# Optimization experiments

Measured on AMD Instinct MI355X. Metric: run time of the kernel, lower is better.

Reference implementation:

```python
import jax, jax.numpy as jnp
import numpy as np

N_NODES = 200000
IN_SIZE = 128
OUT_SIZE = 128
N_EDGES = 600000


def setup_inputs() -> dict:
    key = jax.random.key(0)
    k1, k2, k3, k4 = jax.random.split(key, 4)
    embedding = jax.random.normal(k1, (N_NODES, IN_SIZE), dtype=jnp.float32)
    up2down_edge_index = jax.random.randint(k2, (2, N_EDGES), 0, N_NODES, dtype=jnp.int64)
    # GCNConv params (glorot weight, zero bias as in PyG defaults)
    scale = np.sqrt(6.0 / (IN_SIZE + OUT_SIZE)).astype(np.float32)
    W = jax.random.uniform(k3, (IN_SIZE, OUT_SIZE), dtype=jnp.float32, minval=-scale, maxval=scale)
    b = jnp.zeros((OUT_SIZE,), dtype=jnp.float32)
    return {"embedding": embedding, "up2down_edge_index": up2down_edge_index, "W": W, "b": b}


def reference(embedding, up2down_edge_index, W, b):
    # PyG GCNConv: add self-loops, symmetric normalization, linear transform,
    # scatter-sum aggregation, add bias.
    N = embedding.shape[0]
    loops = jnp.arange(N, dtype=up2down_edge_index.dtype)
    src = jnp.concatenate([up2down_edge_index[0], loops])  # message sources
    dst = jnp.concatenate([up2down_edge_index[1], loops])  # message targets

    # degree of each target node (edge_weight = 1)
    deg = jax.ops.segment_sum(jnp.ones_like(src, dtype=embedding.dtype), dst, num_segments=N)
    deg_inv_sqrt = jnp.where(deg > 0, jax.lax.rsqrt(jnp.maximum(deg, 1.0)), 0.0)
    norm = deg_inv_sqrt[src] * deg_inv_sqrt[dst]  # [E+N]

    h = embedding @ W  # [N, out]
    msg = h[src] * norm[:, None]  # gather + scale, [E+N, out]
    out = jax.ops.segment_sum(msg, dst, num_segments=N)  # scatter-add
    return out + b
```

## Files before the change

### kernel.cpp

```cpp
#include <hip/hip_runtime.h>
#include <hip/hip_bf16.h>
#include <stdint.h>

typedef __attribute__((ext_vector_type(8))) short short8v;
typedef __attribute__((ext_vector_type(4))) float f32x4;

__device__ __forceinline__ unsigned short f2bf(float f) {
  unsigned int u = __float_as_uint(f);
  u += 0x7fffu + ((u >> 16) & 1u);
  return (unsigned short)(u >> 16);
}
__device__ __forceinline__ unsigned int pack2bf(float a, float b) {
  return (unsigned int)f2bf(a) | ((unsigned int)f2bf(b) << 16);
}
__device__ __forceinline__ float bf_lo(unsigned int v) { return __uint_as_float(v << 16); }
__device__ __forceinline__ float bf_hi(unsigned int v) { return __uint_as_float(v & 0xffff0000u); }

__global__ void k_prep(uint4* __restrict__ zp, int n16,
                       const float* __restrict__ W, unsigned short* __restrict__ Wfrag) {
  int b = blockIdx.x;
  if (b < 64) {
    int t = b * 256 + threadIdx.x;
    int j = t & 7;
    int lane = (t >> 3) & 63;
    int ktct = t >> 9;
    int kt = ktct & 3, ct = ktct >> 2;
    int col = ct * 16 + (lane & 15);
    int k = kt * 32 + 4 * (lane >> 4) + (j & 3) + 16 * (j >> 2);
    Wfrag[t] = f2bf(W[k * 128 + col]);
  } else {
    int i = (b - 64) * 256 + threadIdx.x;
    if (i < n16) {
      uint4 z; z.x = z.y = z.z = z.w = 0u;
      zp[i] = z;
    }
  }
}

__global__ void k_count(const int* __restrict__ dst, int* deg, int E) {
  int e = blockIdx.x * blockDim.x + threadIdx.x;
  if (e < E) atomicAdd(&deg[dst[e]], 1);
}

__global__ void k_blocksum(const int* __restrict__ deg, int* partials, float* dis, int N) {
  __shared__ int s[256];
  int t = threadIdx.x;
  int i = blockIdx.x * 256 + t;
  int c = (i < N) ? deg[i] : 0;
  if (i < N) dis[i] = rsqrtf((float)(c + 1));
  s[t] = c;
  __syncthreads();
  for (int off = 128; off > 0; off >>= 1) {
    if (t < off) s[t] += s[t + off];
    __syncthreads();
  }
  if (t == 0) partials[blockIdx.x] = s[0];
}

__global__ void k_scan_final2(const int* __restrict__ deg, const int* __restrict__ partials,
                              int* csr_off, int N, int E) {
  __shared__ int s[256];
  __shared__ int base;
  int t = threadIdx.x;
  int accp = 0;
  for (int j = t; j < blockIdx.x; j += 256) accp += partials[j];
  s[t] = accp;
  __syncthreads();
  for (int off = 128; off > 0; off >>= 1) {
    if (t < off) s[t] += s[t + off];
    __syncthreads();
  }
  if (t == 0) base = s[0];
  __syncthreads();
  int i = blockIdx.x * 256 + t;
  int c = (i < N) ? deg[i] : 0;
  s[t] = c;
  __syncthreads();
  for (int off = 1; off < 256; off <<= 1) {
    int v = (t >= off) ? s[t - off] : 0;
    __syncthreads();
    s[t] += v;
    __syncthreads();
  }
  if (i < N) csr_off[i] = base + s[t] - c;
  if (i == 0) csr_off[N] = E;
}

__global__ void k_fill(const int* __restrict__ src, const int* __restrict__ dst,
                       const int* __restrict__ csr_off, int* cursor, int* csr_src, int E) {
  int e = blockIdx.x * blockDim.x + threadIdx.x;
  if (e < E) {
    int d = dst[e];
    int p = atomicAdd(&cursor[d], 1);
    csr_src[csr_off[d] + p] = src[e];
  }
}

__device__ __forceinline__ short8v pack8(f32x4 a, f32x4 b) {
  short8v r;
  r[0] = (short)f2bf(a[0]); r[1] = (short)f2bf(a[1]);
  r[2] = (short)f2bf(a[2]); r[3] = (short)f2bf(a[3]);
  r[4] = (short)f2bf(b[0]); r[5] = (short)f2bf(b[1]);
  r[6] = (short)f2bf(b[2]); r[7] = (short)f2bf(b[3]);
  return r;
}


#define GLOAD(XB, DD, TT, HAS)                                                  \
  do {                                                                          \
    if (HAS) {                                                                  \
      int row_ = (TT) * 16 + lr;                                                \
      if (row_ < N) {                                                           \
        const float* xp_ = X + (size_t)row_ * 128 + 4 * lg;                     \
        _Pragma("unroll") for (int q = 0; q < 4; ++q) {                         \
          XB[2 * q]     = *(const f32x4*)(xp_ + q * 32);                        \
          XB[2 * q + 1] = *(const f32x4*)(xp_ + q * 32 + 16);                   \
        }                                                                       \
        DD = dis[row_];                                                         \
      } else {                                                                  \
        _Pragma("unroll") for (int q = 0; q < 8; ++q) {                         \
          XB[q][0] = XB[q][1] = XB[q][2] = XB[q][3] = 0.f;                      \
        }                                                                       \
        DD = 0.f;                                                               \
      }                                                                         \
    }                                                                           \
  } while (0)

#define GCOMPUTE(XB, DD, TT)                                                    \
  do {                                                                          \
    short8v afr[4];                                                             \
    _Pragma("unroll") for (int kt = 0; kt < 4; ++kt)                            \
        afr[kt] = pack8(XB[2 * kt], XB[2 * kt + 1]);                            \
    int row_ = (TT) * 16 + lr;                                                  \
    bool wr_ = row_ < N;                                                        \
    unsigned short* hp_ = hs + (size_t)row_ * 128;                              \
    float dd_ = DD;                                                             \
    _Pragma("unroll") for (int cp = 0; cp < 4; ++cp) {                          \
      f32x4 a0 = {0.f, 0.f, 0.f, 0.f}, a1 = {0.f, 0.f, 0.f, 0.f};               \
      _Pragma("unroll") for (int kt = 0; kt < 4; ++kt)                          \
          a0 = __builtin_amdgcn_mfma_f32_16x16x32_bf16(wreg[(2 * cp) * 4 + kt], \
                                                       afr[kt], a0, 0, 0, 0);   \
      _Pragma("unroll") for (int kt = 0; kt < 4; ++kt)                          \
          a1 = __builtin_amdgcn_mfma_f32_16x16x32_bf16(                         \
              wreg[(2 * cp + 1) * 4 + kt], afr[kt], a1, 0, 0, 0);               \
      unsigned int u0x = pack2bf(a0[0] * dd_, a0[1] * dd_);                     \
      unsigned int u0y = pack2bf(a0[2] * dd_, a0[3] * dd_);                     \
      unsigned int u1x = pack2bf(a1[0] * dd_, a1[1] * dd_);                     \
      unsigned int u1y = pack2bf(a1[2] * dd_, a1[3] * dd_);                     \
      int s_ = lg & 1;                                                          \
      unsigned int sx = s_ ? u0x : u1x, sy = s_ ? u0y : u1y;                    \
      unsigned int rx = (unsigned int)__shfl_xor((int)sx, 16);                  \
      unsigned int ry = (unsigned int)__shfl_xor((int)sy, 16);                  \
      uint4 uu;                                                                 \
      if (s_ == 0) { uu.x = u0x; uu.y = u0y; uu.z = rx; uu.w = ry; }            \
      else         { uu.x = rx; uu.y = ry; uu.z = u1x; uu.w = u1y; }            \
      int cb = (s_ ? (2 * cp + 1) : (2 * cp)) * 16 + 8 * (lg >> 1);             \
      if (wr_) *(uint4*)(hp_ + cb) = uu;                                        \
    }                                                                           \
  } while (0)

__global__ __launch_bounds__(256, 2) void k_gemm5(const float* __restrict__ X,
     const unsigned short* __restrict__ Wfrag, const float* __restrict__ dis,
     unsigned short* __restrict__ hs, int N, int ntile) {
  int lane = threadIdx.x & 63;
  int gw = (blockIdx.x * blockDim.x + threadIdx.x) >> 6;
  int nw = (gridDim.x * blockDim.x) >> 6;
  int lr = lane & 15, lg = lane >> 4;

  short8v wreg[32];
  #pragma unroll
  for (int f = 0; f < 32; ++f)
    wreg[f] = *(const short8v*)(Wfrag + (size_t)(f * 64 + lane) * 8);

  int tile = gw;
  if (tile >= ntile) return;

  f32x4 xv[8], nx[8];
  float d0 = 0.f, d1 = 0.f;
  GLOAD(xv, d0, tile, true);

  for (;;) {
    int t1 = tile + nw;
    bool h1 = t1 < ntile;
    GLOAD(nx, d1, t1, h1);
    __builtin_amdgcn_sched_barrier(0);
    GCOMPUTE(xv, d0, tile);
    if (!h1) break;
    int t2 = t1 + nw;
    bool h2 = t2 < ntile;
    GLOAD(xv, d0, t2, h2);
    __builtin_amdgcn_sched_barrier(0);
    GCOMPUTE(nx, d1, t1);
    if (!h2) break;
    tile = t2;
  }
}

__device__ __forceinline__ void acc8(float* a, uint4 g) {
  a[0] += bf_lo(g.x); a[1] += bf_hi(g.x);
  a[2] += bf_lo(g.y); a[3] += bf_hi(g.y);
  a[4] += bf_lo(g.z); a[5] += bf_hi(g.z);
  a[6] += bf_lo(g.w); a[7] += bf_hi(g.w);
}

__global__ __launch_bounds__(256) void k_agg2(const unsigned short* __restrict__ hs_,
     const int* __restrict__ csr_src, const int* __restrict__ csr_off,
     const float* __restrict__ dis, const float* __restrict__ bias,
     float* __restrict__ out, int N) {
  const uint4* hs = (const uint4*)hs_;
  int lane = threadIdx.x & 63;
  int c = lane & 15;
  int base = lane & 48;
  int gid = (blockIdx.x * blockDim.x + threadIdx.x) >> 4;
  int G = (gridDim.x * blockDim.x) >> 4;
  int i0 = (int)(((long long)gid * N) / G);
  int i1 = (int)(((long long)(gid + 1) * N) / G);
  if (i0 >= i1) return;
  float4 bA = ((const float4*)bias)[c * 2];
  float4 bB = ((const float4*)bias)[c * 2 + 1];
  int e1prev = csr_off[i0];
  for (int i = i0; i < i1; ++i) {
    int e0 = e1prev;
    int e1 = csr_off[i + 1];
    e1prev = e1;
    float a[8];
    uint4 sv = hs[(size_t)i * 16 + c];
    a[0] = bf_lo(sv.x); a[1] = bf_hi(sv.x);
    a[2] = bf_lo(sv.y); a[3] = bf_hi(sv.y);
    a[4] = bf_lo(sv.z); a[5] = bf_hi(sv.z);
    a[6] = bf_lo(sv.w); a[7] = bf_hi(sv.w);
    int e = e0;
    while (e < e1) {
      int p = e + c;
      int myidx = (p < e1) ? csr_src[p] : 0;
      int kb = (e1 - e < 16) ? (e1 - e) : 16;
      int k = 0;
      for (; k + 8 <= kb; k += 8) {
        int s[8];
        #pragma unroll
        for (int q = 0; q < 8; ++q) s[q] = __shfl(myidx, base + k + q);
        uint4 g[8];
        #pragma unroll
        for (int q = 0; q < 8; ++q) g[q] = hs[(size_t)s[q] * 16 + c];
        #pragma unroll
        for (int q = 0; q < 8; ++q) acc8(a, g[q]);
      }
      for (; k < kb; k += 4) {
        int s0 = __shfl(myidx, base + k);
        int s1 = __shfl(myidx, base + k + 1);
        int s2 = __shfl(myidx, base + k + 2);
        int s3 = __shfl(myidx, base + k + 3);
        bool v1 = (k + 1 < kb), v2 = (k + 2 < kb), v3 = (k + 3 < kb);
        uint4 g0 = hs[(size_t)s0 * 16 + c];
        uint4 g1 = hs[(size_t)(v1 ? s1 : i) * 16 + c];
        uint4 g2 = hs[(size_t)(v2 ? s2 : i) * 16 + c];
        uint4 g3 = hs[(size_t)(v3 ? s3 : i) * 16 + c];
        if (!v1) { g1.x = g1.y = g1.z = g1.w = 0u; }
        if (!v2) { g2.x = g2.y = g2.z = g2.w = 0u; }
        if (!v3) { g3.x = g3.y = g3.z = g3.w = 0u; }
        acc8(a, g0); acc8(a, g1); acc8(a, g2); acc8(a, g3);
      }
      e += kb;
    }
    float di = dis[i];
    f32x4 o0, o1;
    o0[0] = fmaf(di, a[0], bA.x); o0[1] = fmaf(di, a[1], bA.y);
    o0[2] = fmaf(di, a[2], bA.z); o0[3] = fmaf(di, a[3], bA.w);
    o1[0] = fmaf(di, a[4], bB.x); o1[1] = fmaf(di, a[5], bB.y);
    o1[2] = fmaf(di, a[6], bB.z); o1[3] = fmaf(di, a[7], bB.w);
    f32x4* op = (f32x4*)(out + (size_t)i * 128);
    __builtin_nontemporal_store(o0, op + c * 2);
    __builtin_nontemporal_store(o1, op + c * 2 + 1);
  }
}

extern "C" void kernel_launch(void* const* d_in, const int* in_sizes, int n_in,
                              void* d_out, int out_size, void* d_ws, size_t ws_size,
                              hipStream_t stream) {
  const float* X    = (const float*)d_in[0];
  const int*   edge = (const int*)d_in[1];
  const float* W    = (const float*)d_in[2];
  const float* bias = (const float*)d_in[3];
  float* out = (float*)d_out;
  int N = in_sizes[0] / 128;
  int E = in_sizes[1] / 2;
  const int* srcArr = edge;
  const int* dstArr = edge + E;

  char* w = (char*)d_ws;
  auto align = [](size_t x) { return (x + 255) & ~(size_t)255; };
  size_t o = 0;
  int*   deg      = (int*)(w + o);   o += align((size_t)N * 4);
  int*   cursor   = (int*)(w + o);   o += align((size_t)N * 4);
  float* dis      = (float*)(w + o); o += align((size_t)N * 4);
  int*   csr_off  = (int*)(w + o);   o += align(((size_t)N + 1) * 4);
  int*   csr_src  = (int*)(w + o);   o += align((size_t)E * 4);
  int*   partials = (int*)(w + o);   o += align((size_t)4096 * 4);
  unsigned short* Wfrag = (unsigned short*)(w + o); o += align((size_t)16384 * 2);
  unsigned short* hs    = (unsigned short*)(w + o);

  int nbN = (N + 255) / 256;
  int nbE = (E + 255) / 256;
  int ntile = (N + 15) / 16;

  size_t zbytes = align((size_t)N * 4) + align((size_t)N * 4);
  int n16 = (int)(zbytes / 16);
  k_prep<<<64 + (n16 + 255) / 256, 256, 0, stream>>>((uint4*)deg, n16, W, Wfrag);
  k_count<<<nbE, 256, 0, stream>>>(dstArr, deg, E);
  k_blocksum<<<nbN, 256, 0, stream>>>(deg, partials, dis, N);
  k_scan_final2<<<nbN, 256, 0, stream>>>(deg, partials, csr_off, N, E);
  k_fill<<<nbE, 256, 0, stream>>>(srcArr, dstArr, csr_off, cursor, csr_src, E);
  k_gemm5<<<512, 256, 0, stream>>>(X, Wfrag, dis, hs, N, ntile);
  k_agg2<<<4096, 256, 0, stream>>>(hs, csr_src, csr_off, dis, bias, out, N);
}
```

Baseline: 149.0 us.

## Fuse block-sum into count kernel and triple-buffer GEMM tile loads

The per-block degree partial sums are now built with a second atomic during edge counting, which removes the separate block-sum kernel and one launch. The rsqrt degree normalisation moves into the scan kernel. Partials move into the zeroed workspace region. The GEMM loop changes from double to triple buffering of X tiles to deepen load prefetch, at the cost of more registers and extra contended atomics on the partials array.

```diff
diff --git a/kernel.cpp b/kernel.cpp
--- a/kernel.cpp
+++ b/kernel.cpp
@@ -37,28 +37,17 @@
   }
 }
 
-__global__ void k_count(const int* __restrict__ dst, int* deg, int E) {
+__global__ void k_count2(const int* __restrict__ dst, int* deg, int* partials, int E) {
   int e = blockIdx.x * blockDim.x + threadIdx.x;
-  if (e < E) atomicAdd(&deg[dst[e]], 1);
-}
-
-__global__ void k_blocksum(const int* __restrict__ deg, int* partials, float* dis, int N) {
-  __shared__ int s[256];
-  int t = threadIdx.x;
-  int i = blockIdx.x * 256 + t;
-  int c = (i < N) ? deg[i] : 0;
-  if (i < N) dis[i] = rsqrtf((float)(c + 1));
-  s[t] = c;
-  __syncthreads();
-  for (int off = 128; off > 0; off >>= 1) {
-    if (t < off) s[t] += s[t + off];
-    __syncthreads();
-  }
-  if (t == 0) partials[blockIdx.x] = s[0];
-}
-
-__global__ void k_scan_final2(const int* __restrict__ deg, const int* __restrict__ partials,
-                              int* csr_off, int N, int E) {
+  if (e < E) {
+    int d = dst[e];
+    atomicAdd(&deg[d], 1);
+    atomicAdd(&partials[d >> 8], 1);
+  }
+}
+
+__global__ void k_scan_final3(const int* __restrict__ deg, const int* __restrict__ partials,
+                              int* csr_off, float* __restrict__ dis, int N, int E) {
   __shared__ int s[256];
   __shared__ int base;
   int t = threadIdx.x;
@@ -74,6 +63,7 @@
   __syncthreads();
   int i = blockIdx.x * 256 + t;
   int c = (i < N) ? deg[i] : 0;
+  if (i < N) dis[i] = rsqrtf((float)(c + 1));
   s[t] = c;
   __syncthreads();
   for (int off = 1; off < 256; off <<= 1) {
@@ -172,27 +162,36 @@
   for (int f = 0; f < 32; ++f)
     wreg[f] = *(const short8v*)(Wfrag + (size_t)(f * 64 + lane) * 8);
 
-  int tile = gw;
-  if (tile >= ntile) return;
-
-  f32x4 xv[8], nx[8];
-  float d0 = 0.f, d1 = 0.f;
-  GLOAD(xv, d0, tile, true);
+  int t0 = gw;
+  if (t0 >= ntile) return;
+
+  f32x4 b0[8], b1[8], b2[8];
+  float d0 = 0.f, d1 = 0.f, d2 = 0.f;
+  GLOAD(b0, d0, t0, true);
+  int t1 = t0 + nw;
+  bool h1 = t1 < ntile;
+  GLOAD(b1, d1, t1, h1);
 
   for (;;) {
-    int t1 = tile + nw;
-    bool h1 = t1 < ntile;
-    GLOAD(nx, d1, t1, h1);
-    __builtin_amdgcn_sched_barrier(0);
-    GCOMPUTE(xv, d0, tile);
-    if (!h1) break;
     int t2 = t1 + nw;
     bool h2 = t2 < ntile;
-    GLOAD(xv, d0, t2, h2);
+    GLOAD(b2, d2, t2, h2);
     __builtin_amdgcn_sched_barrier(0);
-    GCOMPUTE(nx, d1, t1);
+    GCOMPUTE(b0, d0, t0);
+    if (!h1) break;
+    int t3 = t2 + nw;
+    bool h3 = t3 < ntile;
+    GLOAD(b0, d0, t3, h3);
+    __builtin_amdgcn_sched_barrier(0);
+    GCOMPUTE(b1, d1, t1);
     if (!h2) break;
-    tile = t2;
+    int t4 = t3 + nw;
+    bool h4 = t4 < ntile;
+    GLOAD(b1, d1, t4, h4);
+    __builtin_amdgcn_sched_barrier(0);
+    GCOMPUTE(b2, d2, t2);
+    if (!h3) break;
+    t0 = t3; t1 = t4; h1 = h4;
   }
 }
 
@@ -292,10 +291,11 @@
   size_t o = 0;
   int*   deg      = (int*)(w + o);   o += align((size_t)N * 4);
   int*   cursor   = (int*)(w + o);   o += align((size_t)N * 4);
+  int*   partials = (int*)(w + o);   o += align((size_t)4096 * 4);
+  size_t zend = o;
   float* dis      = (float*)(w + o); o += align((size_t)N * 4);
   int*   csr_off  = (int*)(w + o);   o += align(((size_t)N + 1) * 4);
   int*   csr_src  = (int*)(w + o);   o += align((size_t)E * 4);
-  int*   partials = (int*)(w + o);   o += align((size_t)4096 * 4);
   unsigned short* Wfrag = (unsigned short*)(w + o); o += align((size_t)16384 * 2);
   unsigned short* hs    = (unsigned short*)(w + o);
 
@@ -303,12 +303,10 @@
   int nbE = (E + 255) / 256;
   int ntile = (N + 15) / 16;
 
-  size_t zbytes = align((size_t)N * 4) + align((size_t)N * 4);
-  int n16 = (int)(zbytes / 16);
-  k_prep<<<64 + (n16 + 255) / 256, 256, 0, stream>>>((uint4*)deg, n16, W, Wfrag);
-  k_count<<<nbE, 256, 0, stream>>>(dstArr, deg, E);
-  k_blocksum<<<nbN, 256, 0, stream>>>(deg, partials, dis, N);
-  k_scan_final2<<<nbN, 256, 0, stream>>>(deg, partials, csr_off, N, E);
+  int n16 = (int)(zend / 16);
+  k_prep<<<64 + (n16 + 255) / 256, 256, 0, stream>>>((uint4*)d_ws, n16, W, Wfrag);
+  k_count2<<<nbE, 256, 0, stream>>>(dstArr, deg, partials, E);
+  k_scan_final3<<<nbN, 256, 0, stream>>>(deg, partials, csr_off, dis, N, E);
   k_fill<<<nbE, 256, 0, stream>>>(srcArr, dstArr, csr_off, cursor, csr_src, E);
   k_gemm5<<<512, 256, 0, stream>>>(X, Wfrag, dis, hs, N, ntile);
   k_agg2<<<4096, 256, 0, stream>>>(hs, csr_src, csr_off, dis, bias, out, N);
```

After: 299.1 us. 101% more time.

## Stage GEMM input tiles into LDS with async global_load_lds double buffering

Applied to the files above, without the earlier changes.

The GEMM kernel now streams 64-row chunks of X into shared memory with direct global-to-LDS loads, double-buffered two chunks ahead, and waits on vmcnt before reading fragments from LDS. Before, each wave loaded its X rows into registers with explicit ping-pong buffers. This is meant to free registers and overlap the bulk fp32 input reads with MFMA work. The grid changes from 512 to 782 blocks. It adds 64KB of LDS per block, which may limit occupancy, and it relies on a hand-written vmcnt wait, where the count of outstanding loads also includes the dis load and the hs stores.

```diff
diff --git a/kernel.cpp b/kernel.cpp
--- a/kernel.cpp
+++ b/kernel.cpp
@@ -4,6 +4,8 @@
 
 typedef __attribute__((ext_vector_type(8))) short short8v;
 typedef __attribute__((ext_vector_type(4))) float f32x4;
+typedef __attribute__((address_space(3))) uint32_t as3_u32;
+typedef const __attribute__((address_space(1))) uint32_t as1_u32;
 
 __device__ __forceinline__ unsigned short f2bf(float f) {
   unsigned int u = __float_as_uint(f);
@@ -105,66 +107,12 @@
   return r;
 }
 
-
-#define GLOAD(XB, DD, TT, HAS)                                                  \
-  do {                                                                          \
-    if (HAS) {                                                                  \
-      int row_ = (TT) * 16 + lr;                                                \
-      if (row_ < N) {                                                           \
-        const float* xp_ = X + (size_t)row_ * 128 + 4 * lg;                     \
-        _Pragma("unroll") for (int q = 0; q < 4; ++q) {                         \
-          XB[2 * q]     = *(const f32x4*)(xp_ + q * 32);                        \
-          XB[2 * q + 1] = *(const f32x4*)(xp_ + q * 32 + 16);                   \
-        }                                                                       \
-        DD = dis[row_];                                                         \
-      } else {                                                                  \
-        _Pragma("unroll") for (int q = 0; q < 8; ++q) {                         \
-          XB[q][0] = XB[q][1] = XB[q][2] = XB[q][3] = 0.f;                      \
-        }                                                                       \
-        DD = 0.f;                                                               \
-      }                                                                         \
-    }                                                                           \
-  } while (0)
-
-#define GCOMPUTE(XB, DD, TT)                                                    \
-  do {                                                                          \
-    short8v afr[4];                                                             \
-    _Pragma("unroll") for (int kt = 0; kt < 4; ++kt)                            \
-        afr[kt] = pack8(XB[2 * kt], XB[2 * kt + 1]);                            \
-    int row_ = (TT) * 16 + lr;                                                  \
-    bool wr_ = row_ < N;                                                        \
-    unsigned short* hp_ = hs + (size_t)row_ * 128;                              \
-    float dd_ = DD;                                                             \
-    _Pragma("unroll") for (int cp = 0; cp < 4; ++cp) {                          \
-      f32x4 a0 = {0.f, 0.f, 0.f, 0.f}, a1 = {0.f, 0.f, 0.f, 0.f};               \
-      _Pragma("unroll") for (int kt = 0; kt < 4; ++kt)                          \
-          a0 = __builtin_amdgcn_mfma_f32_16x16x32_bf16(wreg[(2 * cp) * 4 + kt], \
-                                                       afr[kt], a0, 0, 0, 0);   \
-      _Pragma("unroll") for (int kt = 0; kt < 4; ++kt)                          \
-          a1 = __builtin_amdgcn_mfma_f32_16x16x32_bf16(                         \
-              wreg[(2 * cp + 1) * 4 + kt], afr[kt], a1, 0, 0, 0);               \
-      unsigned int u0x = pack2bf(a0[0] * dd_, a0[1] * dd_);                     \
-      unsigned int u0y = pack2bf(a0[2] * dd_, a0[3] * dd_);                     \
-      unsigned int u1x = pack2bf(a1[0] * dd_, a1[1] * dd_);                     \
-      unsigned int u1y = pack2bf(a1[2] * dd_, a1[3] * dd_);                     \
-      int s_ = lg & 1;                                                          \
-      unsigned int sx = s_ ? u0x : u1x, sy = s_ ? u0y : u1y;                    \
-      unsigned int rx = (unsigned int)__shfl_xor((int)sx, 16);                  \
-      unsigned int ry = (unsigned int)__shfl_xor((int)sy, 16);                  \
-      uint4 uu;                                                                 \
-      if (s_ == 0) { uu.x = u0x; uu.y = u0y; uu.z = rx; uu.w = ry; }            \
-      else         { uu.x = rx; uu.y = ry; uu.z = u1x; uu.w = u1y; }            \
-      int cb = (s_ ? (2 * cp + 1) : (2 * cp)) * 16 + 8 * (lg >> 1);             \
-      if (wr_) *(uint4*)(hp_ + cb) = uu;                                        \
-    }                                                                           \
-  } while (0)
-
-__global__ __launch_bounds__(256, 2) void k_gemm5(const float* __restrict__ X,
+__global__ __launch_bounds__(256, 2) void k_gemm7(const float* __restrict__ X,
      const unsigned short* __restrict__ Wfrag, const float* __restrict__ dis,
-     unsigned short* __restrict__ hs, int N, int ntile) {
-  int lane = threadIdx.x & 63;
-  int gw = (blockIdx.x * blockDim.x + threadIdx.x) >> 6;
-  int nw = (gridDim.x * blockDim.x) >> 6;
+     unsigned short* __restrict__ hs, int N, int nchunk, int grid) {
+  __shared__ float xs[2][4][2048];
+  int tid = threadIdx.x;
+  int wv = tid >> 6, lane = tid & 63;
   int lr = lane & 15, lg = lane >> 4;
 
   short8v wreg[32];
@@ -172,28 +120,70 @@
   for (int f = 0; f < 32; ++f)
     wreg[f] = *(const short8v*)(Wfrag + (size_t)(f * 64 + lane) * 8);
 
-  int tile = gw;
-  if (tile >= ntile) return;
-
-  f32x4 xv[8], nx[8];
-  float d0 = 0.f, d1 = 0.f;
-  GLOAD(xv, d0, tile, true);
-
-  for (;;) {
-    int t1 = tile + nw;
-    bool h1 = t1 < ntile;
-    GLOAD(nx, d1, t1, h1);
+  int c0 = blockIdx.x;
+  if (c0 >= nchunk) return;
+  int colbase = 4 * lg;
+
+#define STAGE7(C, B)                                                            \
+  do {                                                                          \
+    int c_ = (C);                                                               \
+    int row_ = c_ * 64 + wv * 16 + lr;                                          \
+    const float* gb_ =                                                          \
+        X + (size_t)((c_ < nchunk && row_ < N) ? row_ : 0) * 128 + colbase;     \
+    float* rg_ = &xs[B][wv][0];                                                 \
+    _Pragma("unroll") for (int q = 0; q < 8; ++q)                               \
+        __builtin_amdgcn_global_load_lds(                                       \
+            (as1_u32*)(gb_ + (q >> 1) * 32 + (q & 1) * 16),                     \
+            (as3_u32*)(rg_ + q * 256), 16, 0, 0);                               \
+  } while (0)
+
+  STAGE7(c0, 0);
+  STAGE7(c0 + grid, 1);
+  int cur = 0;
+  for (int c = c0; c < nchunk; c += grid) {
+    asm volatile("s_waitcnt vmcnt(8)" ::: "memory");
     __builtin_amdgcn_sched_barrier(0);
-    GCOMPUTE(xv, d0, tile);
-    if (!h1) break;
-    int t2 = t1 + nw;
-    bool h2 = t2 < ntile;
-    GLOAD(xv, d0, t2, h2);
-    __builtin_amdgcn_sched_barrier(0);
-    GCOMPUTE(nx, d1, t1);
-    if (!h2) break;
-    tile = t2;
-  }
+    const float* region = &xs[cur][wv][0];
+    short8v afr[4];
+    #pragma unroll
+    for (int kt = 0; kt < 4; ++kt) {
+      f32x4 lo = *(const f32x4*)(region + (2 * kt) * 256 + lane * 4);
+      f32x4 hi = *(const f32x4*)(region + (2 * kt + 1) * 256 + lane * 4);
+      afr[kt] = pack8(lo, hi);
+    }
+    int row = c * 64 + wv * 16 + lr;
+    bool wr = row < N;
+    float dd = wr ? dis[row] : 0.f;
+    unsigned short* hp = hs + (size_t)row * 128;
+    #pragma unroll
+    for (int cp = 0; cp < 4; ++cp) {
+      f32x4 a0 = {0.f, 0.f, 0.f, 0.f}, a1 = {0.f, 0.f, 0.f, 0.f};
+      #pragma unroll
+      for (int kt = 0; kt < 4; ++kt)
+        a0 = __builtin_amdgcn_mfma_f32_16x16x32_bf16(wreg[(2 * cp) * 4 + kt],
+                                                     afr[kt], a0, 0, 0, 0);
+      #pragma unroll
+      for (int kt = 0; kt < 4; ++kt)
+        a1 = __builtin_amdgcn_mfma_f32_16x16x32_bf16(wreg[(2 * cp + 1) * 4 + kt],
+                                                     afr[kt], a1, 0, 0, 0);
+      unsigned int u0x = pack2bf(a0[0] * dd, a0[1] * dd);
+      unsigned int u0y = pack2bf(a0[2] * dd, a0[3] * dd);
+      unsigned int u1x = pack2bf(a1[0] * dd, a1[1] * dd);
+      unsigned int u1y = pack2bf(a1[2] * dd, a1[3] * dd);
+      int s_ = lg & 1;
+      unsigned int sx = s_ ? u0x : u1x, sy = s_ ? u0y : u1y;
+      unsigned int rx = (unsigned int)__shfl_xor((int)sx, 16);
+      unsigned int ry = (unsigned int)__shfl_xor((int)sy, 16);
+      uint4 uu;
+      if (s_ == 0) { uu.x = u0x; uu.y = u0y; uu.z = rx; uu.w = ry; }
+      else         { uu.x = rx; uu.y = ry; uu.z = u1x; uu.w = u1y; }
+      int cb = (s_ ? (2 * cp + 1) : (2 * cp)) * 16 + 8 * (lg >> 1);
+      if (wr) *(uint4*)(hp + cb) = uu;
+    }
+    STAGE7(c + 2 * grid, cur);
+    cur ^= 1;
+  }
+#undef STAGE7
 }
 
 __device__ __forceinline__ void acc8(float* a, uint4 g) {
@@ -301,7 +291,8 @@
 
   int nbN = (N + 255) / 256;
   int nbE = (E + 255) / 256;
-  int ntile = (N + 15) / 16;
+  int nchunk = (N + 63) / 64;
+  int gridG = 782;
 
   size_t zbytes = align((size_t)N * 4) + align((size_t)N * 4);
   int n16 = (int)(zbytes / 16);
@@ -310,6 +301,6 @@
   k_blocksum<<<nbN, 256, 0, stream>>>(deg, partials, dis, N);
   k_scan_final2<<<nbN, 256, 0, stream>>>(deg, partials, csr_off, N, E);
   k_fill<<<nbE, 256, 0, stream>>>(srcArr, dstArr, csr_off, cursor, csr_src, E);
-  k_gemm5<<<512, 256, 0, stream>>>(X, Wfrag, dis, hs, N, ntile);
+  k_gemm7<<<gridG, 256, 0, stream>>>(X, Wfrag, dis, hs, N, nchunk, gridG);
   k_agg2<<<4096, 256, 0, stream>>>(hs, csr_src, csr_off, dis, bias, out, N);
 }
```

Result: slower. 158.0 us (+6.1%).

## Stage W fragments in LDS instead of registers to raise GEMM occupancy

Applied to the files above, without the earlier changes.

The GEMM kernel now copies the pre-swizzled bf16 weight fragments into 32 KB of shared memory per block. Each MFMA reads its operand from LDS instead of keeping 32 short8 fragments resident in VGPRs. This frees registers, so launch bounds go from 2 to 4 blocks per SM and the grid doubles, aiming for more warps to hide latency on the streaming X loads. The cost is extra LDS read traffic on every MFMA and a per-block staging copy.

```diff
diff --git a/kernel.cpp b/kernel.cpp
--- a/kernel.cpp
+++ b/kernel.cpp
@@ -126,7 +126,7 @@
     }                                                                           \
   } while (0)
 
-#define GCOMPUTE(XB, DD, TT)                                                    \
+#define GCOMPUTE8(XB, DD, TT)                                                   \
   do {                                                                          \
     short8v afr[4];                                                             \
     _Pragma("unroll") for (int kt = 0; kt < 4; ++kt)                            \
@@ -137,12 +137,14 @@
     float dd_ = DD;                                                             \
     _Pragma("unroll") for (int cp = 0; cp < 4; ++cp) {                          \
       f32x4 a0 = {0.f, 0.f, 0.f, 0.f}, a1 = {0.f, 0.f, 0.f, 0.f};               \
-      _Pragma("unroll") for (int kt = 0; kt < 4; ++kt)                          \
-          a0 = __builtin_amdgcn_mfma_f32_16x16x32_bf16(wreg[(2 * cp) * 4 + kt], \
-                                                       afr[kt], a0, 0, 0, 0);   \
-      _Pragma("unroll") for (int kt = 0; kt < 4; ++kt)                          \
-          a1 = __builtin_amdgcn_mfma_f32_16x16x32_bf16(                         \
-              wreg[(2 * cp + 1) * 4 + kt], afr[kt], a1, 0, 0, 0);               \
+      _Pragma("unroll") for (int kt = 0; kt < 4; ++kt) {                        \
+        short8v wf = *(const short8v*)(Wl + (((2 * cp) * 4 + kt) * 64 + lane) * 8); \
+        a0 = __builtin_amdgcn_mfma_f32_16x16x32_bf16(wf, afr[kt], a0, 0, 0, 0); \
+      }                                                                         \
+      _Pragma("unroll") for (int kt = 0; kt < 4; ++kt) {                        \
+        short8v wf = *(const short8v*)(Wl + (((2 * cp + 1) * 4 + kt) * 64 + lane) * 8); \
+        a1 = __builtin_amdgcn_mfma_f32_16x16x32_bf16(wf, afr[kt], a1, 0, 0, 0); \
+      }                                                                         \
       unsigned int u0x = pack2bf(a0[0] * dd_, a0[1] * dd_);                     \
       unsigned int u0y = pack2bf(a0[2] * dd_, a0[3] * dd_);                     \
       unsigned int u1x = pack2bf(a1[0] * dd_, a1[1] * dd_);                     \
@@ -159,18 +161,20 @@
     }                                                                           \
   } while (0)
 
-__global__ __launch_bounds__(256, 2) void k_gemm5(const float* __restrict__ X,
+__global__ __launch_bounds__(256, 4) void k_gemm8(const float* __restrict__ X,
      const unsigned short* __restrict__ Wfrag, const float* __restrict__ dis,
      unsigned short* __restrict__ hs, int N, int ntile) {
-  int lane = threadIdx.x & 63;
-  int gw = (blockIdx.x * blockDim.x + threadIdx.x) >> 6;
+  __shared__ unsigned short Wl[16384];
+  int tid = threadIdx.x;
+  #pragma unroll
+  for (int q = 0; q < 8; ++q)
+    ((uint4*)Wl)[q * 256 + tid] = ((const uint4*)Wfrag)[q * 256 + tid];
+  __syncthreads();
+
+  int lane = tid & 63;
+  int gw = (blockIdx.x * blockDim.x + tid) >> 6;
   int nw = (gridDim.x * blockDim.x) >> 6;
   int lr = lane & 15, lg = lane >> 4;
-
-  short8v wreg[32];
-  #pragma unroll
-  for (int f = 0; f < 32; ++f)
-    wreg[f] = *(const short8v*)(Wfrag + (size_t)(f * 64 + lane) * 8);
 
   int tile = gw;
   if (tile >= ntile) return;
@@ -184,13 +188,13 @@
     bool h1 = t1 < ntile;
     GLOAD(nx, d1, t1, h1);
     __builtin_amdgcn_sched_barrier(0);
-    GCOMPUTE(xv, d0, tile);
+    GCOMPUTE8(xv, d0, tile);
     if (!h1) break;
     int t2 = t1 + nw;
     bool h2 = t2 < ntile;
     GLOAD(xv, d0, t2, h2);
     __builtin_amdgcn_sched_barrier(0);
-    GCOMPUTE(nx, d1, t1);
+    GCOMPUTE8(nx, d1, t1);
     if (!h2) break;
     tile = t2;
   }
@@ -310,6 +314,6 @@
   k_blocksum<<<nbN, 256, 0, stream>>>(deg, partials, dis, N);
   k_scan_final2<<<nbN, 256, 0, stream>>>(deg, partials, csr_off, N, E);
   k_fill<<<nbE, 256, 0, stream>>>(srcArr, dstArr, csr_off, cursor, csr_src, E);
-  k_gemm5<<<512, 256, 0, stream>>>(X, Wfrag, dis, hs, N, ntile);
+  k_gemm8<<<1024, 256, 0, stream>>>(X, Wfrag, dis, hs, N, ntile);
   k_agg2<<<4096, 256, 0, stream>>>(hs, csr_src, csr_off, dis, bias, out, N);
 }
```

New measurement: 149.9 us. No clear change (+0.6%).
